# Performance work log

Measured on AMD Instinct MI355X. Metric: run time of the kernel, lower is better.

Reference implementation:

```python
import jax, jax.numpy as jnp
import numpy as np

MUL = 128
LS = [0, 1, 2]
D1 = [MUL * (2 * l + 1) for l in LS]            # per-irrep dims of x1 / out: 128, 384, 640
D2 = [2 * l + 1 for l in LS]                    # per-irrep dims of x2 (mul=1): 1, 3, 5
O1 = np.concatenate([[0], np.cumsum(D1)])       # offsets into x1 / out
O2 = np.concatenate([[0], np.cumsum(D2)])       # offsets into x2
PATHS = [(l1, l2, lo) for l1 in LS for l2 in LS for lo in LS
         if abs(l1 - l2) <= lo <= l1 + l2]      # 15 sorted 'uvw' instructions
DIM_OUT = int(sum(D1))

def _count():
    # fan-in count per output position: each 'uvw' path adds mul_1*mul_2 = 128
    c = np.zeros(DIM_OUT, dtype=np.float32)
    for (_, _, lo) in PATHS:
        c[O1[lo]:O1[lo] + D1[lo]] += MUL * 1
    return np.maximum(c, 1.0)

COUNT = jnp.asarray(_count())

def setup_inputs() -> dict:
    key = jax.random.key(0)
    ks = jax.random.split(key, 3 + len(PATHS))
    N = 16384
    inp = {
        "x1": jax.random.normal(ks[0], (N, int(sum(D1))), jnp.float32),
        "x2": jax.random.normal(ks[1], (N, int(sum(D2))), jnp.float32),
        "ws": jax.random.normal(ks[2], (len(PATHS), MUL, 1, MUL), jnp.float32),
    }
    for p, (l1, l2, lo) in enumerate(PATHS):
        inp[f"c{p}"] = jax.random.normal(ks[3 + p], (2 * l1 + 1, 2 * l2 + 1, 2 * lo + 1), jnp.float32)
    return inp

def _forward(x1, x2, ws, cs):
    N = x1.shape[0]
    out = jnp.zeros((N, DIM_OUT), x1.dtype)
    for p, (l1, l2, lo) in enumerate(PATHS):
        # s1: [N, mul1, 2l1+1]; s2: [N, mul2=1, 2l2+1]
        s1 = x1[:, int(O1[l1]):int(O1[l1] + D1[l1])].reshape(N, MUL, 2 * l1 + 1)
        s2 = x2[:, int(O2[l2]):int(O2[l2] + D2[l2])].reshape(N, 1, 2 * l2 + 1)
        # weighted CG contraction: ws[p] [u,v,w], cs[p] [i,j,k]
        contrib = jnp.einsum('uvw,ijk,zui,zvj->zwk', ws[p], cs[p], s1, s2)
        out = out.at[:, int(O1[lo]):int(O1[lo] + D1[lo])].add(contrib.reshape(N, D1[lo]))
    # fan-in (component) normalization
    return out / jnp.sqrt(COUNT)

def reference(x1, x2, ws, c0, c1, c2, c3, c4, c5, c6, c7, c8, c9, c10, c11, c12, c13, c14):
    cs = [c0, c1, c2, c3, c4, c5, c6, c7, c8, c9, c10, c11, c12, c13, c14]
    return _forward(x1, x2, ws, cs)
```

## Files before the change

### kernel.cpp

```cpp
#include <hip/hip_runtime.h>
#include <hip/hip_bf16.h>

typedef float f32x4 __attribute__((ext_vector_type(4)));
typedef short bf16x8 __attribute__((ext_vector_type(8)));

#define ZT 16
#define TL_RING 16384
#define YL_BUF 448

constexpr int cL1[15]  = {0,0,0,1,1,1,1,1,1,2,2,2,2,2,2};
constexpr int cL2[15]  = {0,1,2,0,1,1,1,2,2,0,1,1,2,2,2};
constexpr int cLO[15]  = {0,1,2,1,0,1,2,1,2,2,1,2,0,1,2};
constexpr int cCSZ[15] = {1,9,25,9,9,27,45,45,75,25,45,75,25,75,125};
constexpr int cCOFF[15]= {0,1,10,35,44,53,80,125,170,245,270,315,390,415,490};
constexpr int cO1[3] = {0,128,512};
constexpr int cO2[3] = {0,1,4};
constexpr int cX1O[3]= {0,1,4};

constexpr int cSEQ [15] = {2,0,6,4,8,12,9,1,11,3,14,5,13,7,10};
constexpr int cROFF[15] = {0,80,0,80,0,80,0,80,0,80,0,80,0,48,0};

struct CP { const float* p[15]; };

__device__ __forceinline__ ushort f2bf(float f) {
    union { __hip_bfloat16 h; ushort u; } c;
    c.h = __float2bfloat16(f);
    return c.u;
}

__global__ void prep_w(const float* __restrict__ ws, ushort* __restrict__ wb) {
    __shared__ float lds[64 * 132];
    const int p = blockIdx.x;
    const int tid = threadIdx.x;
    const float* src = ws + (size_t)p * 16384;
    ushort* dst = wb + (size_t)p * 16384;
    for (int half = 0; half < 2; ++half) {
        for (int i = tid; i < 8192; i += 256) {
            int u = i >> 7, w = i & 127;
            lds[u * 132 + w] = src[(half * 64 + u) * 128 + w];
        }
        __syncthreads();
        for (int i = tid; i < 8192; i += 256) {
            int w = i >> 6, u = i & 63;
            dst[w * 128 + half * 64 + u] = f2bf(lds[u * 132 + w]);
        }
        __syncthreads();
    }
}

template<int P>
__device__ __forceinline__ void compute_y(int tid, const float* __restrict__ cl,
                                          const float* __restrict__ x2l,
                                          float* __restrict__ ybuf) {
    constexpr int l2 = cL2[P], lo = cLO[P];
    constexpr int d1 = 2*cL1[P]+1, d2 = 2*l2+1, dO = 2*lo+1;
    constexpr int span = d1 * dO;
    constexpr int span_pad = (span + 3) & ~3;
    constexpr int ny = ZT * span_pad;
    for (int idx = tid; idx < ny; idx += 256) {
        const int z = idx / span_pad, rem = idx - z * span_pad;
        float s = 0.f;
        if (rem < span) {
            const int i = rem / dO, k = rem - i * dO;
            #pragma unroll
            for (int j = 0; j < d2; ++j)
                s += cl[cCOFF[P] + (i*d2 + j)*dO + k] * x2l[z*9 + cO2[l2] + j];
        }
        ybuf[idx] = s;
    }
}

template<int S>
__device__ __forceinline__ void path_iter(
    int tid, const ushort* __restrict__ Wb, const float* __restrict__ Wsrc, int use_prep,
    const float (&x1r)[4][2][9],
    float* __restrict__ yl, ushort* __restrict__ Tl,
    const float* __restrict__ cl, const float* __restrict__ x2l,
    f32x4 (&A0)[1][2], f32x4 (&A1)[3][2], f32x4 (&A2)[5][2])
{
    constexpr int P = cSEQ[S];
    constexpr int l1 = cL1[P], lo = cLO[P];
    constexpr int d1 = 2*l1+1, dO = 2*lo+1;
    constexpr int span = d1 * dO;
    constexpr int span_pad = (span + 3) & ~3;
    const int lane = tid & 63, wv = tid >> 6;

    ushort* Tcur = Tl + cROFF[S] * 128;
    const float* ycur = yl + (S & 1) * YL_BUF;

    {
        const int u0 = 2 * lane;
        #pragma unroll
        for (int r = 0; r < 4; ++r) {
            const int z = wv * 4 + r;
            f32x4 yv[span_pad / 4];
            #pragma unroll
            for (int j = 0; j < span_pad / 4; ++j)
                yv[j] = *reinterpret_cast<const f32x4*>(ycur + z * span_pad + 4 * j);
            #pragma unroll
            for (int k = 0; k < dO; ++k) {
                const int col = z * dO + k;
                float s0 = 0.f, s1 = 0.f;
                #pragma unroll
                for (int i = 0; i < d1; ++i) {
                    const int yi = i * dO + k;
                    const float yf = yv[yi >> 2][yi & 3];
                    s0 += x1r[r][0][cX1O[l1] + i] * yf;
                    s1 += x1r[r][1][cX1O[l1] + i] * yf;
                }
                union { uint u32; ushort h[2]; } pk;
                pk.h[0] = f2bf(s0);
                pk.h[1] = f2bf(s1);
                const uint idx = (uint)(col * 128 + u0) ^ (uint)((col & 7) << 3);
                *reinterpret_cast<uint*>(Tcur + idx) = pk.u32;
            }
        }
    }

    bf16x8 aP[2][4];
    if (use_prep) {
        const ushort* wp = Wb + P * 16384;
        #pragma unroll
        for (int nt = 0; nt < 2; ++nt)
        #pragma unroll
        for (int ks = 0; ks < 4; ++ks) {
            const int wrow = wv*32 + nt*16 + (lane & 15);
            const int k0   = ks*32 + ((lane >> 4) << 3);
            aP[nt][ks] = *reinterpret_cast<const bf16x8*>(wp + wrow*128 + k0);
        }
    } else {
        const float* wp = Wsrc + P * 16384;
        #pragma unroll
        for (int nt = 0; nt < 2; ++nt)
        #pragma unroll
        for (int ks = 0; ks < 4; ++ks) {
            const int wrow = wv*32 + nt*16 + (lane & 15);
            const int k0   = ks*32 + ((lane >> 4) << 3);
            bf16x8 v;
            #pragma unroll
            for (int e = 0; e < 8; ++e) v[e] = (short)f2bf(wp[(k0 + e)*128 + wrow]);
            aP[nt][ks] = v;
        }
    }

    if constexpr (S < 14)
        compute_y<cSEQ[S + 1]>(tid, cl, x2l, yl + ((S + 1) & 1) * YL_BUF);

    __syncthreads();

    #pragma unroll
    for (int t = 0; t < dO; ++t) {
        #pragma unroll
        for (int ks = 0; ks < 4; ++ks) {
            const int col = t*16 + (lane & 15);
            const int k0  = ks*32 + ((lane >> 4) << 3);
            const uint idx = (uint)(col * 128 + k0) ^ (uint)((col & 7) << 3);
            const bf16x8 a = *reinterpret_cast<const bf16x8*>(Tcur + idx);
            if constexpr (lo == 0) {
                A0[t][0] = __builtin_amdgcn_mfma_f32_16x16x32_bf16(a, aP[0][ks], A0[t][0], 0,0,0);
                A0[t][1] = __builtin_amdgcn_mfma_f32_16x16x32_bf16(a, aP[1][ks], A0[t][1], 0,0,0);
            } else if constexpr (lo == 1) {
                A1[t][0] = __builtin_amdgcn_mfma_f32_16x16x32_bf16(a, aP[0][ks], A1[t][0], 0,0,0);
                A1[t][1] = __builtin_amdgcn_mfma_f32_16x16x32_bf16(a, aP[1][ks], A1[t][1], 0,0,0);
            } else {
                A2[t][0] = __builtin_amdgcn_mfma_f32_16x16x32_bf16(a, aP[0][ks], A2[t][0], 0,0,0);
                A2[t][1] = __builtin_amdgcn_mfma_f32_16x16x32_bf16(a, aP[1][ks], A2[t][1], 0,0,0);
            }
        }
    }
}

template<int LO, int NTILES>
__device__ __forceinline__ void stage_lo(const f32x4 (&A)[NTILES][2], float* __restrict__ stage,
                                         int c, int wv, int g, int m, float scale)
{
    constexpr int dO = 2*LO + 1;
    #pragma unroll
    for (int t = 0; t < NTILES; ++t)
    #pragma unroll
    for (int r = 0; r < 4; ++r) {
        const int zcol = t*16 + g*4 + r;
        const int z = zcol / dO, k = zcol - z*dO;
        if ((z >> 2) == c) {
            #pragma unroll
            for (int nt = 0; nt < 2; ++nt) {
                const int w = wv*32 + nt*16 + m;
                stage[(z & 3)*1152 + cO1[LO] + w*dO + k] = A[t][nt][r] * scale;
            }
        }
    }
}

__global__ __launch_bounds__(256, 2)
void tp_main(const float* __restrict__ x1, const float* __restrict__ x2,
             const float* __restrict__ wsrc, const ushort* __restrict__ wb,
             int use_prep, CP cp, float* __restrict__ out)
{
    __shared__ __align__(16) ushort Tl[TL_RING];
    __shared__ __align__(16) float yl[2 * YL_BUF];
    __shared__ float cl[615];
    __shared__ float x2l[ZT * 9];

    const int tid = threadIdx.x;
    const int z0 = blockIdx.x * ZT;
    const int lane = tid & 63, wv = tid >> 6;

    #pragma unroll
    for (int p = 0; p < 15; ++p)
        for (int i = tid; i < cCSZ[p]; i += 256) cl[cCOFF[p] + i] = cp.p[p][i];
    for (int i = tid; i < ZT * 9; i += 256) x2l[i] = x2[(size_t)z0 * 9 + i];

    float x1r[4][2][9];
    #pragma unroll
    for (int r = 0; r < 4; ++r) {
        const float* b = x1 + (size_t)(z0 + wv*4 + r) * 1152;
        {
            const float2 t = *reinterpret_cast<const float2*>(b + 2*lane);
            x1r[r][0][0] = t.x; x1r[r][1][0] = t.y;
        }
        {
            float f6[6];
            #pragma unroll
            for (int j = 0; j < 3; ++j) {
                const float2 t = *reinterpret_cast<const float2*>(b + 128 + 6*lane + 2*j);
                f6[2*j] = t.x; f6[2*j + 1] = t.y;
            }
            #pragma unroll
            for (int i = 0; i < 3; ++i) { x1r[r][0][1+i] = f6[i]; x1r[r][1][1+i] = f6[3+i]; }
        }
        {
            float f10[10];
            #pragma unroll
            for (int j = 0; j < 5; ++j) {
                const float2 t = *reinterpret_cast<const float2*>(b + 512 + 10*lane + 2*j);
                f10[2*j] = t.x; f10[2*j + 1] = t.y;
            }
            #pragma unroll
            for (int i = 0; i < 5; ++i) { x1r[r][0][4+i] = f10[i]; x1r[r][1][4+i] = f10[5+i]; }
        }
    }

    f32x4 A0[1][2], A1[3][2], A2[5][2];
    #pragma unroll
    for (int nt = 0; nt < 2; ++nt) {
        A0[0][nt] = (f32x4){0.f, 0.f, 0.f, 0.f};
        #pragma unroll
        for (int t = 0; t < 3; ++t) A1[t][nt] = (f32x4){0.f, 0.f, 0.f, 0.f};
        #pragma unroll
        for (int t = 0; t < 5; ++t) A2[t][nt] = (f32x4){0.f, 0.f, 0.f, 0.f};
    }

    __syncthreads();
    compute_y<cSEQ[0]>(tid, cl, x2l, yl);
    __syncthreads();

    path_iter< 0>(tid, wb, wsrc, use_prep, x1r, yl, Tl, cl, x2l, A0, A1, A2);
    path_iter< 1>(tid, wb, wsrc, use_prep, x1r, yl, Tl, cl, x2l, A0, A1, A2);
    path_iter< 2>(tid, wb, wsrc, use_prep, x1r, yl, Tl, cl, x2l, A0, A1, A2);
    path_iter< 3>(tid, wb, wsrc, use_prep, x1r, yl, Tl, cl, x2l, A0, A1, A2);
    path_iter< 4>(tid, wb, wsrc, use_prep, x1r, yl, Tl, cl, x2l, A0, A1, A2);
    path_iter< 5>(tid, wb, wsrc, use_prep, x1r, yl, Tl, cl, x2l, A0, A1, A2);
    path_iter< 6>(tid, wb, wsrc, use_prep, x1r, yl, Tl, cl, x2l, A0, A1, A2);
    path_iter< 7>(tid, wb, wsrc, use_prep, x1r, yl, Tl, cl, x2l, A0, A1, A2);
    path_iter< 8>(tid, wb, wsrc, use_prep, x1r, yl, Tl, cl, x2l, A0, A1, A2);
    path_iter< 9>(tid, wb, wsrc, use_prep, x1r, yl, Tl, cl, x2l, A0, A1, A2);
    path_iter<10>(tid, wb, wsrc, use_prep, x1r, yl, Tl, cl, x2l, A0, A1, A2);
    path_iter<11>(tid, wb, wsrc, use_prep, x1r, yl, Tl, cl, x2l, A0, A1, A2);
    path_iter<12>(tid, wb, wsrc, use_prep, x1r, yl, Tl, cl, x2l, A0, A1, A2);
    path_iter<13>(tid, wb, wsrc, use_prep, x1r, yl, Tl, cl, x2l, A0, A1, A2);
    path_iter<14>(tid, wb, wsrc, use_prep, x1r, yl, Tl, cl, x2l, A0, A1, A2);

    const int g = lane >> 4, m = lane & 15;
    float* stage = (float*)Tl;
    #pragma unroll
    for (int c = 0; c < 4; ++c) {
        __syncthreads();
        stage_lo<0, 1>(A0, stage, c, wv, g, m, 0.05103103630798288f);
        stage_lo<1, 3>(A1, stage, c, wv, g, m, 0.03608439182435161f);
        stage_lo<2, 5>(A2, stage, c, wv, g, m, 0.03608439182435161f);
        __syncthreads();
        float4* dst = (float4*)(out + (size_t)(z0 + 4*c) * 1152);
        const float4* src = (const float4*)stage;
        #pragma unroll
        for (int it = 0; it < 5; ++it) {
            const int idx = it * 256 + tid;
            if (idx < 1152) dst[idx] = src[idx];
        }
    }
}

extern "C" void kernel_launch(void* const* d_in, const int* in_sizes, int n_in,
                              void* d_out, int out_size, void* d_ws, size_t ws_size,
                              hipStream_t stream) {
    const float* x1 = (const float*)d_in[0];
    const float* x2 = (const float*)d_in[1];
    const float* ws = (const float*)d_in[2];
    CP cp;
    for (int p = 0; p < 15; ++p) cp.p[p] = (const float*)d_in[3 + p];
    float* out = (float*)d_out;

    const int N = in_sizes[0] / 1152;
    const int use_prep = (ws_size >= (size_t)(15 * 128 * 128 * 2)) ? 1 : 0;

    if (use_prep)
        prep_w<<<15, 256, 0, stream>>>(ws, (ushort*)d_ws);
    tp_main<<<N / ZT, 256, 0, stream>>>(x1, x2, ws, (const ushort*)d_ws,
                                        use_prep, cp, out);
}
```

Before: 114.7 us.

## Group paths by l1 and load x1 slices lazily to cut register pressure

The path order is changed so all paths sharing the same l1 run back to back. Each l1 slice of x1 is loaded into a 5-wide register buffer only when l1 changes, instead of keeping all 9 components per row resident for the whole kernel. The freed registers allow launch bounds to be raised from 2 to 3 blocks per SIMD for more occupancy. In exchange, x1 global loads now happen mid-pipeline, which can add latency between paths, and the T ring offsets had to be recomputed for the new order.

```diff
diff --git a/kernel.cpp b/kernel.cpp
--- a/kernel.cpp
+++ b/kernel.cpp
@@ -15,10 +15,9 @@
 constexpr int cCOFF[15]= {0,1,10,35,44,53,80,125,170,245,270,315,390,415,490};
 constexpr int cO1[3] = {0,128,512};
 constexpr int cO2[3] = {0,1,4};
-constexpr int cX1O[3]= {0,1,4};
-
-constexpr int cSEQ [15] = {2,0,6,4,8,12,9,1,11,3,14,5,13,7,10};
-constexpr int cROFF[15] = {0,80,0,80,0,80,0,80,0,80,0,80,0,48,0};
+
+constexpr int cSEQ [15] = {2,1,0, 6,3,4,8,5,7, 9,10,11,12,13,14};
+constexpr int cROFF[15] = {0,80,0, 48,0,112,0,80,0, 48,0,48,0,80,0};
 
 struct CP { const float* p[15]; };
 
@@ -70,10 +69,42 @@
     }
 }
 
+template<int L1>
+__device__ __forceinline__ void load_x1(const float* __restrict__ x1, int z0,
+                                        int wv, int lane, float (&x1c)[4][2][5]) {
+    #pragma unroll
+    for (int r = 0; r < 4; ++r) {
+        const float* b = x1 + (size_t)(z0 + wv*4 + r) * 1152;
+        if constexpr (L1 == 0) {
+            const float2 t = *reinterpret_cast<const float2*>(b + 2*lane);
+            x1c[r][0][0] = t.x; x1c[r][1][0] = t.y;
+        } else if constexpr (L1 == 1) {
+            float f6[6];
+            #pragma unroll
+            for (int j = 0; j < 3; ++j) {
+                const float2 t = *reinterpret_cast<const float2*>(b + 128 + 6*lane + 2*j);
+                f6[2*j] = t.x; f6[2*j + 1] = t.y;
+            }
+            #pragma unroll
+            for (int i = 0; i < 3; ++i) { x1c[r][0][i] = f6[i]; x1c[r][1][i] = f6[3+i]; }
+        } else {
+            float f10[10];
+            #pragma unroll
+            for (int j = 0; j < 5; ++j) {
+                const float2 t = *reinterpret_cast<const float2*>(b + 512 + 10*lane + 2*j);
+                f10[2*j] = t.x; f10[2*j + 1] = t.y;
+            }
+            #pragma unroll
+            for (int i = 0; i < 5; ++i) { x1c[r][0][i] = f10[i]; x1c[r][1][i] = f10[5+i]; }
+        }
+    }
+}
+
 template<int S>
 __device__ __forceinline__ void path_iter(
-    int tid, const ushort* __restrict__ Wb, const float* __restrict__ Wsrc, int use_prep,
-    const float (&x1r)[4][2][9],
+    int tid, const float* __restrict__ x1, int z0,
+    const ushort* __restrict__ Wb, const float* __restrict__ Wsrc, int use_prep,
+    float (&x1c)[4][2][5],
     float* __restrict__ yl, ushort* __restrict__ Tl,
     const float* __restrict__ cl, const float* __restrict__ x2l,
     f32x4 (&A0)[1][2], f32x4 (&A1)[3][2], f32x4 (&A2)[5][2])
@@ -88,6 +119,9 @@
     ushort* Tcur = Tl + cROFF[S] * 128;
     const float* ycur = yl + (S & 1) * YL_BUF;
 
+    if constexpr (S == 0 || cL1[cSEQ[S - 1]] != l1)
+        load_x1<l1>(x1, z0, wv, lane, x1c);
+
     {
         const int u0 = 2 * lane;
         #pragma unroll
@@ -105,8 +139,8 @@
                 for (int i = 0; i < d1; ++i) {
                     const int yi = i * dO + k;
                     const float yf = yv[yi >> 2][yi & 3];
-                    s0 += x1r[r][0][cX1O[l1] + i] * yf;
-                    s1 += x1r[r][1][cX1O[l1] + i] * yf;
+                    s0 += x1c[r][0][i] * yf;
+                    s1 += x1c[r][1][i] * yf;
                 }
                 union { uint u32; ushort h[2]; } pk;
                 pk.h[0] = f2bf(s0);
@@ -191,7 +225,7 @@
     }
 }
 
-__global__ __launch_bounds__(256, 2)
+__global__ __launch_bounds__(256, 3)
 void tp_main(const float* __restrict__ x1, const float* __restrict__ x2,
              const float* __restrict__ wsrc, const ushort* __restrict__ wb,
              int use_prep, CP cp, float* __restrict__ out)
@@ -210,35 +244,7 @@
         for (int i = tid; i < cCSZ[p]; i += 256) cl[cCOFF[p] + i] = cp.p[p][i];
     for (int i = tid; i < ZT * 9; i += 256) x2l[i] = x2[(size_t)z0 * 9 + i];
 
-    float x1r[4][2][9];
-    #pragma unroll
-    for (int r = 0; r < 4; ++r) {
-        const float* b = x1 + (size_t)(z0 + wv*4 + r) * 1152;
-        {
-            const float2 t = *reinterpret_cast<const float2*>(b + 2*lane);
-            x1r[r][0][0] = t.x; x1r[r][1][0] = t.y;
-        }
-        {
-            float f6[6];
-            #pragma unroll
-            for (int j = 0; j < 3; ++j) {
-                const float2 t = *reinterpret_cast<const float2*>(b + 128 + 6*lane + 2*j);
-                f6[2*j] = t.x; f6[2*j + 1] = t.y;
-            }
-            #pragma unroll
-            for (int i = 0; i < 3; ++i) { x1r[r][0][1+i] = f6[i]; x1r[r][1][1+i] = f6[3+i]; }
-        }
-        {
-            float f10[10];
-            #pragma unroll
-            for (int j = 0; j < 5; ++j) {
-                const float2 t = *reinterpret_cast<const float2*>(b + 512 + 10*lane + 2*j);
-                f10[2*j] = t.x; f10[2*j + 1] = t.y;
-            }
-            #pragma unroll
-            for (int i = 0; i < 5; ++i) { x1r[r][0][4+i] = f10[i]; x1r[r][1][4+i] = f10[5+i]; }
-        }
-    }
+    float x1c[4][2][5];
 
     f32x4 A0[1][2], A1[3][2], A2[5][2];
     #pragma unroll
@@ -254,21 +260,21 @@
     compute_y<cSEQ[0]>(tid, cl, x2l, yl);
     __syncthreads();
 
-    path_iter< 0>(tid, wb, wsrc, use_prep, x1r, yl, Tl, cl, x2l, A0, A1, A2);
-    path_iter< 1>(tid, wb, wsrc, use_prep, x1r, yl, Tl, cl, x2l, A0, A1, A2);
-    path_iter< 2>(tid, wb, wsrc, use_prep, x1r, yl, Tl, cl, x2l, A0, A1, A2);
-    path_iter< 3>(tid, wb, wsrc, use_prep, x1r, yl, Tl, cl, x2l, A0, A1, A2);
-    path_iter< 4>(tid, wb, wsrc, use_prep, x1r, yl, Tl, cl, x2l, A0, A1, A2);
-    path_iter< 5>(tid, wb, wsrc, use_prep, x1r, yl, Tl, cl, x2l, A0, A1, A2);
-    path_iter< 6>(tid, wb, wsrc, use_prep, x1r, yl, Tl, cl, x2l, A0, A1, A2);
-    path_iter< 7>(tid, wb, wsrc, use_prep, x1r, yl, Tl, cl, x2l, A0, A1, A2);
-    path_iter< 8>(tid, wb, wsrc, use_prep, x1r, yl, Tl, cl, x2l, A0, A1, A2);
-    path_iter< 9>(tid, wb, wsrc, use_prep, x1r, yl, Tl, cl, x2l, A0, A1, A2);
-    path_iter<10>(tid, wb, wsrc, use_prep, x1r, yl, Tl, cl, x2l, A0, A1, A2);
-    path_iter<11>(tid, wb, wsrc, use_prep, x1r, yl, Tl, cl, x2l, A0, A1, A2);
-    path_iter<12>(tid, wb, wsrc, use_prep, x1r, yl, Tl, cl, x2l, A0, A1, A2);
-    path_iter<13>(tid, wb, wsrc, use_prep, x1r, yl, Tl, cl, x2l, A0, A1, A2);
-    path_iter<14>(tid, wb, wsrc, use_prep, x1r, yl, Tl, cl, x2l, A0, A1, A2);
+    path_iter< 0>(tid, x1, z0, wb, wsrc, use_prep, x1c, yl, Tl, cl, x2l, A0, A1, A2);
+    path_iter< 1>(tid, x1, z0, wb, wsrc, use_prep, x1c, yl, Tl, cl, x2l, A0, A1, A2);
+    path_iter< 2>(tid, x1, z0, wb, wsrc, use_prep, x1c, yl, Tl, cl, x2l, A0, A1, A2);
+    path_iter< 3>(tid, x1, z0, wb, wsrc, use_prep, x1c, yl, Tl, cl, x2l, A0, A1, A2);
+    path_iter< 4>(tid, x1, z0, wb, wsrc, use_prep, x1c, yl, Tl, cl, x2l, A0, A1, A2);
+    path_iter< 5>(tid, x1, z0, wb, wsrc, use_prep, x1c, yl, Tl, cl, x2l, A0, A1, A2);
+    path_iter< 6>(tid, x1, z0, wb, wsrc, use_prep, x1c, yl, Tl, cl, x2l, A0, A1, A2);
+    path_iter< 7>(tid, x1, z0, wb, wsrc, use_prep, x1c, yl, Tl, cl, x2l, A0, A1, A2);
+    path_iter< 8>(tid, x1, z0, wb, wsrc, use_prep, x1c, yl, Tl, cl, x2l, A0, A1, A2);
+    path_iter< 9>(tid, x1, z0, wb, wsrc, use_prep, x1c, yl, Tl, cl, x2l, A0, A1, A2);
+    path_iter<10>(tid, x1, z0, wb, wsrc, use_prep, x1c, yl, Tl, cl, x2l, A0, A1, A2);
+    path_iter<11>(tid, x1, z0, wb, wsrc, use_prep, x1c, yl, Tl, cl, x2l, A0, A1, A2);
+    path_iter<12>(tid, x1, z0, wb, wsrc, use_prep, x1c, yl, Tl, cl, x2l, A0, A1, A2);
+    path_iter<13>(tid, x1, z0, wb, wsrc, use_prep, x1c, yl, Tl, cl, x2l, A0, A1, A2);
+    path_iter<14>(tid, x1, z0, wb, wsrc, use_prep, x1c, yl, Tl, cl, x2l, A0, A1, A2);
 
     const int g = lane >> 4, m = lane & 15;
     float* stage = (float*)Tl;
```

After: 311.2 us. 171% more time.
